# Optimization experiments

Hardware: AMD Instinct MI355X
Metric: run time of the kernel (lower is better)

## Reference

```python
import jax, jax.numpy as jnp
import numpy as np

POLY_DEGREE = 3


def setup_inputs() -> dict:
    key = jax.random.key(0)
    k1, k2, k3 = jax.random.split(key, 3)
    B, L, D = 8192, 16, 4096
    total = sum(L ** d for d in range(POLY_DEGREE + 1))  # 4369
    z = jax.random.normal(k1, (B, L), dtype=jnp.float32)
    W = jax.random.normal(k2, (total, D), dtype=jnp.float32) * 0.02
    b = jax.random.normal(k3, (D,), dtype=jnp.float32) * 0.02
    return {"z": z, "W": W, "b": b}


def poly_features(z):
    # Batched equivalent of per-sample torch.kron chain:
    # degree 0 -> [1]; degree k -> kron(deg_{k-1} feature, z) per sample.
    B = z.shape[0]
    feats = [jnp.ones((B, 1), dtype=z.dtype)]
    cur = z  # degree 1
    feats.append(cur)
    for _ in range(2, POLY_DEGREE + 1):
        # kron(out, latent): (i, j) -> out_i * latent_j
        cur = (cur[:, :, None] * z[:, None, :]).reshape(B, -1)
        feats.append(cur)
    return jnp.concatenate(feats, axis=1)  # [B, total_poly_terms]


def reference(z, W, b):
    x = poly_features(z)          # [B, T]
    return x @ W + b              # [B, data_dim]
```

## Files before the change

### kernel.cpp

```cpp
#include <hip/hip_runtime.h>
#include <hip/hip_bf16.h>

#define NDIM  4096
#define MROWS 8192
#define PREAL 969
#define KP    1088
#define NT    17
#define NWFOLD 1088

typedef unsigned short u16;
typedef __attribute__((ext_vector_type(8))) __bf16 bf16x8;
typedef __attribute__((ext_vector_type(8))) u16 u16x8;
typedef __attribute__((ext_vector_type(4))) float f32x4;

__device__ __forceinline__ u16 bf16rne(float f) {
  unsigned int u = __builtin_bit_cast(unsigned int, f);
  u += 0x7fffu + ((u >> 16) & 1u);
  return (u16)(u >> 16);
}

struct Tbl { int v[KP]; };
constexpr Tbl make_table() {
  Tbl t{};
  for (int p = 0; p < KP; ++p) t.v[p] = -1;
  int p = 0;
  t.v[p++] = (16 << 10) | (16 << 5) | 16;
  for (int i = 0; i < 16; ++i) t.v[p++] = (i << 10) | (16 << 5) | 16;
  for (int i = 0; i < 16; ++i)
    for (int j = i; j < 16; ++j) t.v[p++] = (i << 10) | (j << 5) | 16;
  for (int i = 0; i < 16; ++i)
    for (int j = i; j < 16; ++j)
      for (int k = j; k < 16; ++k) t.v[p++] = (i << 10) | (j << 5) | k;
  return t;
}
__device__ constexpr Tbl TBL = make_table();

__global__ void prep_kernel(const float* __restrict__ z, const float* __restrict__ W,
                            const float* __restrict__ bias,
                            u16* __restrict__ xb, u16* __restrict__ wfbt) {
  __shared__ float tile[64][65];
  __shared__ float zs[17];
  const int bx = blockIdx.x;
  const int tid = threadIdx.x;

  if (bx < NWFOLD) {
    const int p0 = (bx % 17) * 64;
    const int d0 = (bx / 17) * 64;
    const int d4 = (tid & 15) * 4;
    const int rb = tid >> 4;
    const int dd = d0 + d4;
#pragma unroll
    for (int pp = 0; pp < 4; ++pp) {
      const int r = pp * 16 + rb;
      const int p = p0 + r;
      const int enc = TBL.v[p];
      f32x4 v = {0.f, 0.f, 0.f, 0.f};
      if (enc >= 0) {
        const int i = enc >> 10, j = (enc >> 5) & 31, k = enc & 31;
        if (k == 16) {
          if (j == 16) {
            if (i == 16) {
              v = *reinterpret_cast<const f32x4*>(W + dd);
              f32x4 bb = *reinterpret_cast<const f32x4*>(bias + dd);
              v.x += bb.x; v.y += bb.y; v.z += bb.z; v.w += bb.w;
            } else {
              v = *reinterpret_cast<const f32x4*>(W + (size_t)(1 + i) * NDIM + dd);
            }
          } else {
            v = *reinterpret_cast<const f32x4*>(W + (size_t)(17 + i * 16 + j) * NDIM + dd);
            if (i != j) {
              f32x4 w2 = *reinterpret_cast<const f32x4*>(W + (size_t)(17 + j * 16 + i) * NDIM + dd);
              v.x += w2.x; v.y += w2.y; v.z += w2.z; v.w += w2.w;
            }
          }
        } else {
          int rows[6];
          int nr = 0;
          rows[nr++] = 273 + i * 256 + j * 16 + k;
          if (i == j && j == k) {
          } else if (i == j) {
            rows[nr++] = 273 + i * 256 + k * 16 + i;
            rows[nr++] = 273 + k * 256 + i * 16 + i;
          } else if (j == k) {
            rows[nr++] = 273 + j * 256 + i * 16 + j;
            rows[nr++] = 273 + j * 256 + j * 16 + i;
          } else {
            rows[nr++] = 273 + i * 256 + k * 16 + j;
            rows[nr++] = 273 + j * 256 + i * 16 + k;
            rows[nr++] = 273 + j * 256 + k * 16 + i;
            rows[nr++] = 273 + k * 256 + i * 16 + j;
            rows[nr++] = 273 + k * 256 + j * 16 + i;
          }
          v = *reinterpret_cast<const f32x4*>(W + (size_t)rows[0] * NDIM + dd);
          for (int s = 1; s < nr; ++s) {
            f32x4 w2 = *reinterpret_cast<const f32x4*>(W + (size_t)rows[s] * NDIM + dd);
            v.x += w2.x; v.y += w2.y; v.z += w2.z; v.w += w2.w;
          }
        }
      }
#pragma unroll
      for (int jj = 0; jj < 4; ++jj) tile[r][d4 + jj] = v[jj];
    }
    __syncthreads();
#pragma unroll
    for (int round = 0; round < 2; ++round) {
      const int v = round * 256 + tid;
      const int d = v >> 3;
      const int tg = v & 7;
      u16x8 pack;
#pragma unroll
      for (int e = 0; e < 8; ++e) pack[e] = bf16rne(tile[tg * 8 + e][d]);
      *reinterpret_cast<u16x8*>(wfbt + (size_t)(d0 + d) * KP + p0 + tg * 8) = pack;
    }
  } else {
    const int row = bx - NWFOLD;
    if (tid < 16) zs[tid] = z[row * 16 + tid];
    if (tid == 16) zs[16] = 1.0f;
    __syncthreads();
    u16* xrow = xb + (size_t)row * KP;
    for (int g = tid; g < KP / 8; g += 256) {
      u16x8 pack;
#pragma unroll
      for (int e = 0; e < 8; ++e) {
        const int enc = TBL.v[g * 8 + e];
        float v = 0.0f;
        if (enc >= 0) v = zs[enc >> 10] * (zs[(enc >> 5) & 31] * zs[enc & 31]);
        pack[e] = bf16rne(v);
      }
      *reinterpret_cast<u16x8*>(xrow + g * 8) = pack;
    }
  }
}

#define GLOAD(gp, lp)                                                                     \
  __builtin_amdgcn_global_load_lds((const __attribute__((address_space(1))) unsigned int*)(gp), \
                                   (__attribute__((address_space(3))) unsigned int*)(lp), 16, 0, 0)

__device__ __forceinline__ void bar() {
  asm volatile("" ::: "memory");
  __builtin_amdgcn_s_barrier();
  asm volatile("" ::: "memory");
}

__global__ __launch_bounds__(512, 2) void gemm_kernel(const u16* __restrict__ xb,
                                                      const u16* __restrict__ wbt,
                                                      float* __restrict__ out) {
  __shared__ u16 lds[2 * 32768];

  const int bid  = blockIdx.x;
  const int xcd  = bid & 7;
  const int idx  = bid >> 3;
  const int mtl  = (idx >> 3) & 3;
  const int ntl  = (idx & 7) | ((idx >> 5) << 3);
  const int brow = (xcd * 4 + mtl) * 256;
  const int bcol = ntl * 256;

  const int tid  = threadIdx.x;
  const int lane = tid & 63;
  const int wid  = tid >> 6;
  const int wr   = wid >> 2;
  const int wc   = wid & 3;
  const int f    = lane & 15;
  const int q    = lane >> 4;
  const int f7   = f & 7;

  const int srow0 = wid * 16 + (lane >> 3);
  const int srow1 = srow0 + 8;
  const u16* gA0 = xb  + (size_t)(brow + srow0) * KP + ((lane & 7) ^ (srow0 & 7)) * 8;
  const u16* gA1 = xb  + (size_t)(brow + srow1) * KP + ((lane & 7) ^ (srow1 & 7)) * 8;
  const u16* gB0 = wbt + (size_t)(bcol + srow0) * KP + ((lane & 7) ^ (srow0 & 7)) * 8;
  const u16* gB1 = wbt + (size_t)(bcol + srow1) * KP + ((lane & 7) ^ (srow1 & 7)) * 8;
  const int dst0 = wid * 1024;
  const int dst1 = dst0 + 512;

#define STGH(U, H) do {                                                              \
    u16* _lb = lds + ((U) & 1) * 32768 + ((H) < 2 ? 0 : 16384) + ((H) & 1) * 8192;   \
    size_t _ko = (size_t)(U) * 64 + (size_t)((H) & 1) * 128 * KP;                    \
    if ((H) < 2) { GLOAD(gA0 + _ko, _lb + dst0); GLOAD(gA1 + _ko, _lb + dst1); }     \
    else         { GLOAD(gB0 + _ko, _lb + dst0); GLOAD(gB1 + _ko, _lb + dst1); }     \
  } while (0)

#define RD_A(mi, kk) (*reinterpret_cast<const bf16x8*>(bufA + (wr * 128 + (mi) * 16 + f) * 64 + (((kk) * 4 + q) ^ f7) * 8))
#define RD_B(ni, kk) (*reinterpret_cast<const bf16x8*>(bufB + (wc * 64 + (ni) * 16 + f) * 64 + (((kk) * 4 + q) ^ f7) * 8))

#define RDA4(MOFF) do {                                                              \
    _Pragma("unroll") for (int _i = 0; _i < 4; ++_i) {                               \
      a_[_i][0] = RD_A((MOFF) + _i, 0); a_[_i][1] = RD_A((MOFF) + _i, 1); }          \
  } while (0)
#define RDB2(NOFF) do {                                                              \
    _Pragma("unroll") for (int _i = 0; _i < 2; ++_i) {                               \
      b_[(NOFF) + _i][0] = RD_B((NOFF) + _i, 0); b_[(NOFF) + _i][1] = RD_B((NOFF) + _i, 1); } \
  } while (0)

#define QUAD(MOFF, NOFF) do {                                                        \
    __builtin_amdgcn_s_setprio(1);                                                   \
    _Pragma("unroll") for (int _m = 0; _m < 4; ++_m)                                 \
    _Pragma("unroll") for (int _n = 0; _n < 2; ++_n)                                 \
    _Pragma("unroll") for (int _k = 0; _k < 2; ++_k)                                 \
      acc[(MOFF) + _m][(NOFF) + _n] = __builtin_amdgcn_mfma_f32_16x16x32_bf16(       \
          a_[_m][_k], b_[(NOFF) + _n][_k], acc[(MOFF) + _m][(NOFF) + _n], 0, 0, 0);  \
    __builtin_amdgcn_s_setprio(0);                                                   \
  } while (0)

  f32x4 acc[8][4] = {};
  bf16x8 a_[4][2], b_[4][2];
  const u16 *bufA, *bufB;

  STGH(0, 0); STGH(0, 1); STGH(0, 2); STGH(0, 3);
  STGH(1, 0);
  asm volatile("s_waitcnt vmcnt(2)" ::: "memory");
  bar();

  for (int t = 0; t < NT - 1; t += 2) {
    bufA = lds; bufB = lds + 16384;
    RDA4(0); RDB2(0);
    STGH(t + 1, 1);
    bar(); QUAD(0, 0); bar();

    RDB2(2);
    STGH(t + 1, 2);
    bar(); QUAD(0, 2); bar();

    RDA4(4);
    STGH(t + 1, 3);
    bar(); QUAD(4, 2); bar();

    STGH(t + 2, 0);
    asm volatile("s_waitcnt vmcnt(2)" ::: "memory");
    bar(); QUAD(4, 0); bar();

    bufA = lds + 32768; bufB = bufA + 16384;
    RDA4(0); RDB2(0);
    STGH(t + 2, 1);
    bar(); QUAD(0, 0); bar();

    RDB2(2);
    STGH(t + 2, 2);
    bar(); QUAD(0, 2); bar();

    RDA4(4);
    STGH(t + 2, 3);
    bar(); QUAD(4, 2); bar();

    if (t + 3 < NT) {
      STGH(t + 3, 0);
      asm volatile("s_waitcnt vmcnt(2)" ::: "memory");
    } else {
      asm volatile("s_waitcnt vmcnt(0)" ::: "memory");
    }
    bar(); QUAD(4, 0); bar();
  }

  bufA = lds; bufB = lds + 16384;
  RDA4(0); RDB2(0); QUAD(0, 0);
  RDB2(2);          QUAD(0, 2);
  RDA4(4);          QUAD(4, 2); QUAD(4, 0);

  const int r0 = brow + wr * 128 + q * 4;
  const int c0 = bcol + wc * 64 + f;
#pragma unroll
  for (int mi = 0; mi < 8; ++mi)
#pragma unroll
    for (int ni = 0; ni < 4; ++ni) {
#pragma unroll
      for (int j = 0; j < 4; ++j)
        out[(size_t)(r0 + mi * 16 + j) * NDIM + (c0 + ni * 16)] = acc[mi][ni][j];
    }
}

__global__ void fallback_kernel(const float* __restrict__ z, const float* __restrict__ W,
                                const float* __restrict__ bias, float* __restrict__ out) {
  __shared__ float feat[4369];
  const int row = blockIdx.x;
  const int tid = threadIdx.x;
  for (int t = tid; t < 4369; t += 256) {
    float v;
    if (t == 0) v = 1.0f;
    else if (t < 17) v = z[row * 16 + t - 1];
    else if (t < 273) { int u = t - 17; v = z[row * 16 + (u >> 4)] * z[row * 16 + (u & 15)]; }
    else { int u = t - 273; v = z[row * 16 + ((u >> 8) & 15)] * (z[row * 16 + ((u >> 4) & 15)] * z[row * 16 + (u & 15)]); }
    feat[t] = v;
  }
  __syncthreads();
  float acc[16];
#pragma unroll
  for (int j = 0; j < 16; ++j) acc[j] = bias[tid + 256 * j];
  for (int t = 0; t < 4369; ++t) {
    const float fv = feat[t];
    const float* wrow = W + (size_t)t * NDIM;
#pragma unroll
    for (int j = 0; j < 16; ++j) acc[j] = fmaf(fv, wrow[tid + 256 * j], acc[j]);
  }
  float* orow = out + (size_t)row * NDIM;
#pragma unroll
  for (int j = 0; j < 16; ++j) orow[tid + 256 * j] = acc[j];
}

extern "C" void kernel_launch(void* const* d_in, const int* in_sizes, int n_in,
                              void* d_out, int out_size, void* d_ws, size_t ws_size,
                              hipStream_t stream) {
  const float* z = (const float*)d_in[0];
  const float* W = (const float*)d_in[1];
  const float* b = (const float*)d_in[2];
  float* out = (float*)d_out;

  const size_t xb_elems  = (size_t)MROWS * KP;
  const size_t wbt_elems = (size_t)NDIM * KP;
  const size_t need = (xb_elems + wbt_elems) * sizeof(u16);

  if (ws_size >= need) {
    u16* xb  = (u16*)d_ws;
    u16* wbt = xb + xb_elems;
    prep_kernel<<<NWFOLD + MROWS, 256, 0, stream>>>(z, W, b, xb, wbt);
    gemm_kernel<<<(MROWS / 256) * (NDIM / 256), 512, 0, stream>>>(xb, wbt, out);
  } else {
    fallback_kernel<<<MROWS, 256, 0, stream>>>(z, W, b, out);
  }
}
```

Measured before the change: 107.0 us.

## Shrink padded K to 1024 and restructure GEMM prefetch into quarter-tile stages

Reduces the padded reduction dimension from 1088 to 1024 (16 K-tiles instead of 17), so the GEMM streams fewer padding columns while still covering the 969 real polynomial terms. It also rewrites the LDS staging so each wave loads row groups matched to the quarter of the tile consumed in each MFMA phase, with vmcnt(4) waits spread through the tile body. The final iteration issues dummy loads of tile 0 to keep the loop uniform, which adds a little wasted bandwidth. The changed row-to-wave mapping and wait counts risk read-before-load hazards if the accounting is wrong.

Measured after the change: 104.3 us. -2.6%, faster.

```diff
diff --git a/kernel.cpp b/kernel.cpp
--- a/kernel.cpp
+++ b/kernel.cpp
@@ -4,9 +4,9 @@
 #define NDIM  4096
 #define MROWS 8192
 #define PREAL 969
-#define KP    1088
-#define NT    17
-#define NWFOLD 1088
+#define KP    1024
+#define NT    16
+#define NWFOLD 1024
 
 typedef unsigned short u16;
 typedef __attribute__((ext_vector_type(8))) __bf16 bf16x8;
@@ -44,8 +44,8 @@
   const int tid = threadIdx.x;
 
   if (bx < NWFOLD) {
-    const int p0 = (bx % 17) * 64;
-    const int d0 = (bx / 17) * 64;
+    const int p0 = (bx & 15) * 64;
+    const int d0 = (bx >> 4) * 64;
     const int d4 = (tid & 15) * 4;
     const int rb = tid >> 4;
     const int dd = d0 + d4;
@@ -142,6 +142,8 @@
   asm volatile("" ::: "memory");
 }
 
+#define VM4 asm volatile("s_waitcnt vmcnt(4)" ::: "memory")
+
 __global__ __launch_bounds__(512, 2) void gemm_kernel(const u16* __restrict__ xb,
                                                       const u16* __restrict__ wbt,
                                                       float* __restrict__ out) {
@@ -164,20 +166,16 @@
   const int q    = lane >> 4;
   const int f7   = f & 7;
 
-  const int srow0 = wid * 16 + (lane >> 3);
-  const int srow1 = srow0 + 8;
-  const u16* gA0 = xb  + (size_t)(brow + srow0) * KP + ((lane & 7) ^ (srow0 & 7)) * 8;
-  const u16* gA1 = xb  + (size_t)(brow + srow1) * KP + ((lane & 7) ^ (srow1 & 7)) * 8;
-  const u16* gB0 = wbt + (size_t)(bcol + srow0) * KP + ((lane & 7) ^ (srow0 & 7)) * 8;
-  const u16* gB1 = wbt + (size_t)(bcol + srow1) * KP + ((lane & 7) ^ (srow1 & 7)) * 8;
-  const int dst0 = wid * 1024;
-  const int dst1 = dst0 + 512;
-
-#define STGH(U, H) do {                                                              \
-    u16* _lb = lds + ((U) & 1) * 32768 + ((H) < 2 ? 0 : 16384) + ((H) & 1) * 8192;   \
-    size_t _ko = (size_t)(U) * 64 + (size_t)((H) & 1) * 128 * KP;                    \
-    if ((H) < 2) { GLOAD(gA0 + _ko, _lb + dst0); GLOAD(gA1 + _ko, _lb + dst1); }     \
-    else         { GLOAD(gB0 + _ko, _lb + dst0); GLOAD(gB1 + _ko, _lb + dst1); }     \
+  const int lr = lane >> 3;
+  const int swzc = ((lane & 7) ^ lr) * 8;
+  const u16* gA = xb  + (size_t)(brow + lr) * KP + swzc;
+  const u16* gB = wbt + (size_t)(bcol + lr) * KP + swzc;
+  const int aB0 = (wid >> 2) * 128 + (wid & 3) * 16;
+  const int bB0 = (wid >> 1) * 64 + (wid & 1) * 16;
+
+#define STGQ(gptr, region, rb, U) do {                                               \
+    GLOAD((gptr) + (size_t)(rb) * KP + (U) * 64, (region) + (rb) * 64);              \
+    GLOAD((gptr) + (size_t)((rb) + 8) * KP + (U) * 64, (region) + ((rb) + 8) * 64);  \
   } while (0)
 
 #define RD_A(mi, kk) (*reinterpret_cast<const bf16x8*>(bufA + (wr * 128 + (mi) * 16 + f) * 64 + (((kk) * 4 + q) ^ f7) * 8))
@@ -202,59 +200,35 @@
     __builtin_amdgcn_s_setprio(0);                                                   \
   } while (0)
 
+#define TILE_BODY(cA, cB, nA, nB, U) do {                                            \
+    bufA = (cA); bufB = (cB);                                                        \
+    RDA4(0); RDB2(0); STGQ(gA, (nA), aB0, (U));                                      \
+    bar(); QUAD(0, 0); VM4; bar();                                                   \
+    RDB2(2);          STGQ(gB, (nB), bB0, (U));                                      \
+    bar(); QUAD(0, 2); VM4; bar();                                                   \
+    RDA4(4);          STGQ(gB, (nB), bB0 + 32, (U));                                 \
+    bar(); QUAD(4, 2); bar();                                                        \
+                      STGQ(gA, (nA), aB0 + 64, (U));                                 \
+    bar(); QUAD(4, 0); VM4; bar();                                                   \
+  } while (0)
+
   f32x4 acc[8][4] = {};
   bf16x8 a_[4][2], b_[4][2];
   const u16 *bufA, *bufB;
 
-  STGH(0, 0); STGH(0, 1); STGH(0, 2); STGH(0, 3);
-  STGH(1, 0);
-  asm volatile("s_waitcnt vmcnt(2)" ::: "memory");
-  bar();
-
-  for (int t = 0; t < NT - 1; t += 2) {
-    bufA = lds; bufB = lds + 16384;
-    RDA4(0); RDB2(0);
-    STGH(t + 1, 1);
-    bar(); QUAD(0, 0); bar();
-
-    RDB2(2);
-    STGH(t + 1, 2);
-    bar(); QUAD(0, 2); bar();
-
-    RDA4(4);
-    STGH(t + 1, 3);
-    bar(); QUAD(4, 2); bar();
-
-    STGH(t + 2, 0);
-    asm volatile("s_waitcnt vmcnt(2)" ::: "memory");
-    bar(); QUAD(4, 0); bar();
-
-    bufA = lds + 32768; bufB = bufA + 16384;
-    RDA4(0); RDB2(0);
-    STGH(t + 2, 1);
-    bar(); QUAD(0, 0); bar();
-
-    RDB2(2);
-    STGH(t + 2, 2);
-    bar(); QUAD(0, 2); bar();
-
-    RDA4(4);
-    STGH(t + 2, 3);
-    bar(); QUAD(4, 2); bar();
-
-    if (t + 3 < NT) {
-      STGH(t + 3, 0);
-      asm volatile("s_waitcnt vmcnt(2)" ::: "memory");
-    } else {
-      asm volatile("s_waitcnt vmcnt(0)" ::: "memory");
-    }
-    bar(); QUAD(4, 0); bar();
-  }
-
-  bufA = lds; bufB = lds + 16384;
-  RDA4(0); RDB2(0); QUAD(0, 0);
-  RDB2(2);          QUAD(0, 2);
-  RDA4(4);          QUAD(4, 2); QUAD(4, 0);
+  u16* b0A = lds;            u16* b0B = lds + 16384;
+  u16* b1A = lds + 32768;    u16* b1B = b1A + 16384;
+
+  STGQ(gA, b0A, aB0, 0); STGQ(gB, b0B, bB0, 0);
+  STGQ(gB, b0B, bB0 + 32, 0); STGQ(gA, b0A, aB0 + 64, 0);
+  VM4; bar();
+
+  for (int t = 0; t < NT; t += 2) {
+    const int u2 = (t + 2 < NT) ? (t + 2) : 0;
+    TILE_BODY(b0A, b0B, b1A, b1B, t + 1);
+    TILE_BODY(b1A, b1B, b0A, b0B, u2);
+  }
+  asm volatile("s_waitcnt vmcnt(0)" ::: "memory");
 
   const int r0 = brow + wr * 128 + q * 4;
   const int c0 = bcol + wc * 64 + f;
```
